# Kernel tuning notes

Hardware: AMD Instinct MI355X
Metric: run time of the kernel (lower is better)

The kernel has to match this reference:

```python
import jax, jax.numpy as jnp
import numpy as np

IMG_W, IMG_H = 512, 512      # cfg.NETWORK.IMAGE_SIZE
HM_W, HM_H = 128, 128        # cfg.NETWORK.HEATMAP_SIZE
CUBE = (64, 64, 64)          # cube_size (voxel resolution)
N_VIEWS, BATCH, N_JOINTS = 5, 4, 15


def setup_inputs() -> dict:
    key = jax.random.key(0)
    k1, k2, k3 = jax.random.split(key, 3)
    heatmaps = jax.random.uniform(k1, (N_VIEWS, BATCH, N_JOINTS, HM_H, HM_W), jnp.float32)
    projM = jax.random.normal(k2, (N_VIEWS, BATCH, 3, 4), jnp.float32)
    grid_center = jax.random.normal(k3, (BATCH, 3), jnp.float32)
    return {"heatmaps": heatmaps, "projM": projM, "grid_center": grid_center, "grid_size": 8000}


def _compute_grid(grid_size, center):
    # torch.linspace(-s/2, s/2, n) + center[d], meshgrid 'ij' -> flattened [P, 3]
    half = jnp.float32(grid_size) * 0.5
    axes = [jnp.linspace(-half, half, n) + center[d] for d, n in enumerate(CUBE)]
    gx, gy, gz = jnp.meshgrid(*axes, indexing="ij")
    return jnp.stack([gx.ravel(), gy.ravel(), gz.ravel()], axis=-1)


def _bilinear(img, coords):
    # img: [J, H, W]; coords: [P, 2] normalized to [-1, 1], align_corners=True, zero padding
    J, H, W = img.shape
    ix = (coords[:, 0] + 1.0) * 0.5 * (W - 1)
    iy = (coords[:, 1] + 1.0) * 0.5 * (H - 1)
    x0 = jnp.floor(ix); y0 = jnp.floor(iy)
    x1 = x0 + 1.0;      y1 = y0 + 1.0
    wx1 = ix - x0; wx0 = 1.0 - wx1
    wy1 = iy - y0; wy0 = 1.0 - wy1

    def corner(xf, yf, w):
        valid = ((xf >= 0) & (xf <= W - 1) & (yf >= 0) & (yf <= H - 1)).astype(img.dtype)
        xi = jnp.clip(xf, 0, W - 1).astype(jnp.int32)
        yi = jnp.clip(yf, 0, H - 1).astype(jnp.int32)
        return img[:, yi, xi] * (w * valid)[None, :]  # [J, P]

    return (corner(x0, y0, wx0 * wy0) + corner(x1, y0, wx1 * wy0)
            + corner(x0, y1, wx0 * wy1) + corner(x1, y1, wx1 * wy1))


def reference(heatmaps, projM, grid_center, grid_size):
    n, B, J, H, W = heatmaps.shape
    dt = heatmaps.dtype
    # world-space voxel grids, one per batch sample: [B, P, 3]
    grids = jax.vmap(lambda c: _compute_grid(grid_size, c))(grid_center)
    P = grids.shape[1]
    # project_pose_sync takes grid with axes permuted [x, z, y]; pinhole 3x4 projection + perspective divide
    pts = grids[:, :, jnp.array([0, 2, 1])]
    homog = jnp.concatenate([pts, jnp.ones_like(pts[..., :1])], axis=-1)  # [B, P, 4]
    proj = jnp.einsum("nbij,bpj->nbpi", projM, homog)                     # [n, B, P, 3]
    xy = proj[..., :2] / proj[..., 2:3]                                   # [n, B, P, 2]
    # visibility mask per view
    inb = ((xy[..., 0] >= 0) & (xy[..., 1] >= 0)
           & (xy[..., 0] < IMG_W) & (xy[..., 1] < IMG_H)).astype(dt)      # [n, B, P]
    xy = jnp.clip(xy, -1.0, float(max(IMG_W, IMG_H)))
    xy = xy * jnp.array([HM_W / IMG_W, HM_H / IMG_H], dt)
    sg = jnp.clip(xy / jnp.array([HM_W - 1, HM_H - 1], dt) * 2.0 - 1.0, -1.1, 1.1)
    # bilinear grid_sample over all (view, batch) pairs at once
    samp = jax.vmap(_bilinear)(heatmaps.reshape(n * B, J, H, W),
                               sg.reshape(n * B, P, 2))                   # [n*B, J, P]
    samp = samp.reshape(n, B, J, P)
    num = jnp.einsum("nbjp,nbp->bjp", samp, inb)
    den = jnp.sum(inb, axis=0) + 1e-6                                     # [B, P]
    cubes = num / den[:, None, :]
    cubes = jnp.clip(jnp.where(jnp.isnan(cubes), 0.0, cubes), 0.0, 1.0)
    cubes = cubes.reshape(B, J, *CUBE)
    return cubes, grids
```

## Files before the change

kernel.cpp:

```cpp
#include <hip/hip_runtime.h>
#include <hip/hip_fp16.h>

#define NV 5
#define NB 4
#define NJ 15
#define HMW 128
#define HMH 128
#define P_TOTAL (64 * 64 * 64)
#define HM_PLANE (HMH * HMW)
#define CUBES_ELEMS ((size_t)NB * NJ * P_TOTAL)
#define N_PLANES (NV * NB * NJ)
#define QUAD_BYTES ((size_t)N_PLANES * HM_PLANE * 8)

struct __align__(8) H4 { __half2 r0, r1; };
struct F2 { float x, y; };

__global__ __launch_bounds__(256) void build_quads(
    const float* __restrict__ hm, H4* __restrict__ q)
{
    const int idx = blockIdx.x * 256 + threadIdx.x;
    const int pix = idx & (HM_PLANE - 1);
    const int pl  = idx >> 14;
    const int y   = pix >> 7;
    const int x   = pix & 127;
    const float* img = hm + (size_t)pl * HM_PLANE;
    const int x1 = (x < 127) ? x + 1 : 127;
    const int y1 = (y < 127) ? y + 1 : 127;
    const float v00 = img[y  * HMW + x], v01 = img[y  * HMW + x1];
    const float v10 = img[y1 * HMW + x], v11 = img[y1 * HMW + x1];
    H4 h;
    h.r0 = __floats2half2_rn(v00, v01);
    h.r1 = __floats2half2_rn(v10, v11);
    q[idx] = h;
}

__global__ __launch_bounds__(256) void project_layer_tiled(
    const H4*  __restrict__ quads,
    const float* __restrict__ projM,
    const float* __restrict__ center,
    const int*   __restrict__ gsize,
    float* __restrict__ out)
{
    __shared__ float xpose[NJ + 3][256];

    const int blk = blockIdx.x;
    const int b   = blk >> 10;
    const int ib  = (blk >> 6) & 15;
    const int jb  = (blk >> 2) & 15;
    const int kb  = blk & 3;

    const int t  = threadIdx.x;
    const int w  = t >> 6;
    const int l  = t & 63;
    const int di = l >> 4;
    const int dj = (l >> 2) & 3;
    const int dk = l & 3;

    const int gi = ib * 4 + di;
    const int gj = jb * 4 + dj;
    const int gk = kb * 16 + w * 4 + dk;

    const float gs   = (float)gsize[0];
    const float half = gs * 0.5f;
    const float step = gs / 63.0f;

    const float cx = center[b * 3 + 0];
    const float cy = center[b * 3 + 1];
    const float cz = center[b * 3 + 2];

    const float gx = ((gi == 63) ? half : fmaf((float)gi, step, -half)) + cx;
    const float gy = ((gj == 63) ? half : fmaf((float)gj, step, -half)) + cy;
    const float gz = ((gk == 63) ? half : fmaf((float)gk, step, -half)) + cz;

    float num[NJ];
#pragma unroll
    for (int j = 0; j < NJ; ++j) num[j] = 0.0f;
    float cnt = 0.0f;

    for (int n = 0; n < NV; ++n) {
        const float* M = projM + ((size_t)(n * NB + b)) * 12;
        const float px = M[0] * gx + M[1] * gz + M[2]  * gy + M[3];
        const float py = M[4] * gx + M[5] * gz + M[6]  * gy + M[7];
        const float pz = M[8] * gx + M[9] * gz + M[10] * gy + M[11];

        const float u = px / pz;
        const float v = py / pz;

        const bool inb = (u >= 0.0f) && (v >= 0.0f) && (u < 512.0f) && (v < 512.0f);
        if (!inb) continue;

        cnt += 1.0f;

        const float ix = u * 0.25f;
        const float iy = v * 0.25f;

        const float x0f = floorf(ix);
        const float y0f = floorf(iy);
        const float wx1 = ix - x0f, wx0 = 1.0f - wx1;
        const float wy1 = iy - y0f, wy0 = 1.0f - wy1;

        const int x0 = (int)x0f;
        const int y0 = (int)y0f;

        const float wx1v = (x0 < 127) ? wx1 : 0.0f;
        const float wy1v = (y0 < 127) ? wy1 : 0.0f;

        const float w00 = wx0  * wy0;
        const float w01 = wx1v * wy0;
        const float w10 = wx0  * wy1v;
        const float w11 = wx1v * wy1v;

        const int o = y0 * HMW + x0;
        const H4* qb = quads + ((size_t)(n * NB + b) * NJ) * HM_PLANE + o;
#pragma unroll
        for (int j = 0; j < NJ; ++j) {
            const H4 qd = qb[(size_t)j * HM_PLANE];
            const float2 f0 = __half22float2(qd.r0);
            const float2 f1 = __half22float2(qd.r1);
            num[j] += w00 * f0.x + w01 * f0.y + w10 * f1.x + w11 * f1.y;
        }
    }

    const float den = cnt + 1e-6f;
    const float r   = 1.0f / den;

    const int f = di * 64 + dj * 16 + w * 4 + dk;
    const int s = f ^ (((f >> 6) & 3) << 2);
#pragma unroll
    for (int j = 0; j < NJ; ++j)
        xpose[j][s] = fminf(fmaxf(num[j] * r, 0.0f), 1.0f);
    xpose[NJ + 0][s] = gx;
    xpose[NJ + 1][s] = gy;
    xpose[NJ + 2][s] = gz;
    __syncthreads();

    const int k2 = t & 15, j2 = (t >> 4) & 3, i2 = t >> 6;
    const int s2 = t ^ (((t >> 6) & 3) << 2);
    const int p  = (ib * 4 + i2) * 4096 + (jb * 4 + j2) * 64 + kb * 16 + k2;

    {
        float* cb = out + (size_t)b * NJ * P_TOTAL + p;
#pragma unroll
        for (int j = 0; j < NJ; ++j)
            __builtin_nontemporal_store(xpose[j][s2], &cb[(size_t)j * P_TOTAL]);
    }
    {
        float* go = out + CUBES_ELEMS + ((size_t)b * P_TOTAL + p) * 3;
        __builtin_nontemporal_store(xpose[NJ + 0][s2], &go[0]);
        __builtin_nontemporal_store(xpose[NJ + 1][s2], &go[1]);
        __builtin_nontemporal_store(xpose[NJ + 2][s2], &go[2]);
    }
}

__global__ __launch_bounds__(256) void project_layer_fallback(
    const float* __restrict__ hm,
    const float* __restrict__ projM,
    const float* __restrict__ center,
    const int*   __restrict__ gsize,
    float* __restrict__ out)
{
    const int blk = blockIdx.x;
    const int b   = blk >> 10;
    const int p   = ((blk & 1023) << 8) | threadIdx.x;
    const int gi  = p >> 12;
    const int gj  = (p >> 6) & 63;
    const int gk  = p & 63;

    const float gs   = (float)gsize[0];
    const float half = gs * 0.5f;
    const float step = gs / 63.0f;

    const float cx = center[b * 3 + 0];
    const float cy = center[b * 3 + 1];
    const float cz = center[b * 3 + 2];

    const float gx = ((gi == 63) ? half : fmaf((float)gi, step, -half)) + cx;
    const float gy = ((gj == 63) ? half : fmaf((float)gj, step, -half)) + cy;
    const float gz = ((gk == 63) ? half : fmaf((float)gk, step, -half)) + cz;

    float num[NJ];
#pragma unroll
    for (int j = 0; j < NJ; ++j) num[j] = 0.0f;
    float cnt = 0.0f;

    for (int n = 0; n < NV; ++n) {
        const float* M = projM + ((size_t)(n * NB + b)) * 12;
        const float px = M[0] * gx + M[1] * gz + M[2]  * gy + M[3];
        const float py = M[4] * gx + M[5] * gz + M[6]  * gy + M[7];
        const float pz = M[8] * gx + M[9] * gz + M[10] * gy + M[11];
        const float u = px / pz;
        const float v = py / pz;
        const bool inb = (u >= 0.0f) && (v >= 0.0f) && (u < 512.0f) && (v < 512.0f);
        if (!inb) continue;
        cnt += 1.0f;
        const float ix = u * 0.25f;
        const float iy = v * 0.25f;
        const float x0f = floorf(ix);
        const float y0f = floorf(iy);
        const float wx1 = ix - x0f, wx0 = 1.0f - wx1;
        const float wy1 = iy - y0f, wy0 = 1.0f - wy1;
        const int x0 = (int)x0f;
        const int y0 = (int)y0f;
        const bool  xe = (x0 == 127);
        const float wA = xe ? 0.0f : wx0;
        const float wB = xe ? wx0  : wx1;
        const float wy1v = (y0 <= 126) ? wy1 : 0.0f;
        const float wA0 = wA * wy0;
        const float wB0 = wB * wy0;
        const float wA1 = wA * wy1v;
        const float wB1 = wB * wy1v;
        const int xb  = xe ? 126 : x0;
        const int yr1 = (y0 <= 126) ? (y0 + 1) : 127;
        const int o0  = y0  * HMW + xb;
        const int o1  = yr1 * HMW + xb;
        const float* img = hm + ((size_t)(n * NB + b) * NJ) * HM_PLANE;
#pragma unroll
        for (int j = 0; j < NJ; ++j) {
            const float* ij = img + (size_t)j * HM_PLANE;
            const F2 r0 = *(const F2*)(ij + o0);
            const F2 r1 = *(const F2*)(ij + o1);
            num[j] += wA0 * r0.x + wB0 * r0.y + wA1 * r1.x + wB1 * r1.y;
        }
    }

    const float den = cnt + 1e-6f;
    const float r   = 1.0f / den;
    {
        float* cb = out + (size_t)b * NJ * P_TOTAL + p;
#pragma unroll
        for (int j = 0; j < NJ; ++j) {
            const float c = num[j] * r;
            __builtin_nontemporal_store(fminf(fmaxf(c, 0.0f), 1.0f),
                                        &cb[(size_t)j * P_TOTAL]);
        }
    }
    {
        float* go = out + CUBES_ELEMS + ((size_t)b * P_TOTAL + p) * 3;
        __builtin_nontemporal_store(gx, &go[0]);
        __builtin_nontemporal_store(gy, &go[1]);
        __builtin_nontemporal_store(gz, &go[2]);
    }
}

extern "C" void kernel_launch(void* const* d_in, const int* in_sizes, int n_in,
                              void* d_out, int out_size, void* d_ws, size_t ws_size,
                              hipStream_t stream) {
    const float* hm     = (const float*)d_in[0];
    const float* projM  = (const float*)d_in[1];
    const float* center = (const float*)d_in[2];
    const int*   gsize  = (const int*)d_in[3];
    float* out = (float*)d_out;

    const int blocks = NB * 1024;

    if (ws_size >= QUAD_BYTES) {
        H4* quads = (H4*)d_ws;
        const int qthreads = N_PLANES * HM_PLANE;
        build_quads<<<qthreads / 256, 256, 0, stream>>>(hm, quads);
        project_layer_tiled<<<blocks, 256, 0, stream>>>(quads, projM, center, gsize, out);
    } else {
        project_layer_fallback<<<blocks, 256, 0, stream>>>(hm, projM, center, gsize, out);
    }
}
```

Baseline: 42.09 us.

## Tile quad texel layout into 4x2 blocks and batch per-view gathers branch-free

The precomputed half-precision quad array is now stored in 4x2 pixel tiles, so neighbouring projected voxels tend to hit the same cache lines. The projection loop first computes per-view weights and offsets for all five views branch-free, with out-of-bounds views getting zero weight and offset 0. A second fully unrolled loop then issues all gathers, so loads from different views can be in flight together and lanes no longer diverge on the in-bounds test. In exchange, every lane now loads for every view, including invalid ones, and more registers are held live.

```diff
diff --git a/kernel.cpp b/kernel.cpp
--- a/kernel.cpp
+++ b/kernel.cpp
@@ -15,14 +15,17 @@
 struct __align__(8) H4 { __half2 r0, r1; };
 struct F2 { float x, y; };
 
-__global__ __launch_bounds__(256) void build_quads(
+__global__ __launch_bounds__(256) void build_quads_tiled(
     const float* __restrict__ hm, H4* __restrict__ q)
 {
     const int idx = blockIdx.x * 256 + threadIdx.x;
-    const int pix = idx & (HM_PLANE - 1);
+    const int qi  = idx & (HM_PLANE - 1);
     const int pl  = idx >> 14;
-    const int y   = pix >> 7;
-    const int x   = pix & 127;
+    const int within = qi & 7;
+    const int tile   = qi >> 3;
+    const int x = (tile & 31) * 4 + (within & 3);
+    const int y = (tile >> 5) * 2 + (within >> 2);
+
     const float* img = hm + (size_t)pl * HM_PLANE;
     const int x1 = (x < 127) ? x + 1 : 127;
     const int y1 = (y < 127) ? y + 1 : 127;
@@ -72,11 +75,11 @@
     const float gy = ((gj == 63) ? half : fmaf((float)gj, step, -half)) + cy;
     const float gz = ((gk == 63) ? half : fmaf((float)gk, step, -half)) + cz;
 
-    float num[NJ];
-#pragma unroll
-    for (int j = 0; j < NJ; ++j) num[j] = 0.0f;
+    float vw00[NV], vw01[NV], vw10[NV], vw11[NV];
+    int   voff[NV];
     float cnt = 0.0f;
 
+#pragma unroll
     for (int n = 0; n < NV; ++n) {
         const float* M = projM + ((size_t)(n * NB + b)) * 12;
         const float px = M[0] * gx + M[1] * gz + M[2]  * gy + M[3];
@@ -87,9 +90,6 @@
         const float v = py / pz;
 
         const bool inb = (u >= 0.0f) && (v >= 0.0f) && (u < 512.0f) && (v < 512.0f);
-        if (!inb) continue;
-
-        cnt += 1.0f;
 
         const float ix = u * 0.25f;
         const float iy = v * 0.25f;
@@ -105,13 +105,24 @@
         const float wx1v = (x0 < 127) ? wx1 : 0.0f;
         const float wy1v = (y0 < 127) ? wy1 : 0.0f;
 
-        const float w00 = wx0  * wy0;
-        const float w01 = wx1v * wy0;
-        const float w10 = wx0  * wy1v;
-        const float w11 = wx1v * wy1v;
-
-        const int o = y0 * HMW + x0;
-        const H4* qb = quads + ((size_t)(n * NB + b) * NJ) * HM_PLANE + o;
+        vw00[n] = inb ? (wx0  * wy0 ) : 0.0f;
+        vw01[n] = inb ? (wx1v * wy0 ) : 0.0f;
+        vw10[n] = inb ? (wx0  * wy1v) : 0.0f;
+        vw11[n] = inb ? (wx1v * wy1v) : 0.0f;
+
+        const int qi = (((y0 >> 1) * 32 + (x0 >> 2)) << 3) | ((y0 & 1) << 2) | (x0 & 3);
+        voff[n] = inb ? qi : 0;
+        cnt += inb ? 1.0f : 0.0f;
+    }
+
+    float num[NJ];
+#pragma unroll
+    for (int j = 0; j < NJ; ++j) num[j] = 0.0f;
+
+#pragma unroll
+    for (int n = 0; n < NV; ++n) {
+        const H4* qb = quads + ((size_t)(n * NB + b) * NJ) * HM_PLANE + voff[n];
+        const float w00 = vw00[n], w01 = vw01[n], w10 = vw10[n], w11 = vw11[n];
 #pragma unroll
         for (int j = 0; j < NJ; ++j) {
             const H4 qd = qb[(size_t)j * HM_PLANE];
@@ -256,7 +267,7 @@
     if (ws_size >= QUAD_BYTES) {
         H4* quads = (H4*)d_ws;
         const int qthreads = N_PLANES * HM_PLANE;
-        build_quads<<<qthreads / 256, 256, 0, stream>>>(hm, quads);
+        build_quads_tiled<<<qthreads / 256, 256, 0, stream>>>(hm, quads);
         project_layer_tiled<<<blocks, 256, 0, stream>>>(quads, projM, center, gsize, out);
     } else {
         project_layer_fallback<<<blocks, 256, 0, stream>>>(hm, projM, center, gsize, out);
```

New measurement: 58.89 us. 1.4x slower.
